# Kernel optimization log

Measured on AMD Instinct MI355X. Metric: run time of the kernel, lower is better.

Reference implementation:

```python
import jax, jax.numpy as jnp
import numpy as np

B, L, N, C = 8, 33600, 128, 80
ALPHA, BETA, TOPK, EPS = 1.0, 6.0, 13, 1e-9


def setup_inputs() -> dict:
    key = jax.random.key(0)
    ks = jax.random.split(key, 7)
    pred_scores = jax.random.uniform(ks[0], (B, L, C), jnp.float32)  # post-sigmoid scores
    pc = jax.random.uniform(ks[1], (B, L, 2), jnp.float32) * 1024.0
    pwh = jax.random.uniform(ks[2], (B, L, 2), jnp.float32) * 128.0 + 8.0
    pred_boxes = jnp.concatenate([pc - pwh / 2, pc + pwh / 2], axis=-1)  # xyxy
    gc = jax.random.uniform(ks[3], (B, N, 2), jnp.float32) * 1024.0
    gwh = jax.random.uniform(ks[4], (B, N, 2), jnp.float32) * 256.0 + 16.0
    gt_boxes = jnp.concatenate([gc - gwh / 2, gc + gwh / 2], axis=-1)  # xyxy
    anchor_points = jax.random.uniform(ks[5], (1, L, 2), jnp.float32) * 1024.0
    gt_labels = jax.random.randint(ks[6], (B, N, 1), 0, C).astype(jnp.int64)
    # last quarter of GT slots are padding
    pad_gt_mask = (jnp.arange(N)[None, :, None] < 96).astype(jnp.float32)
    pad_gt_mask = jnp.broadcast_to(pad_gt_mask, (B, N, 1))
    return {"pred_scores": pred_scores, "pred_boxes": pred_boxes,
            "anchor_points": anchor_points, "gt_labels": gt_labels,
            "gt_boxes": gt_boxes, "pad_gt_mask": pad_gt_mask, "bg_index": C}


def _pairwise_iou(gt, pr):
    # gt: [B,N,4], pr: [B,L,4] xyxy -> iou [B,N,L]
    lt = jnp.maximum(gt[:, :, None, :2], pr[:, None, :, :2])
    rb = jnp.minimum(gt[:, :, None, 2:], pr[:, None, :, 2:])
    wh = jnp.clip(rb - lt, 0.0)
    inter = wh[..., 0] * wh[..., 1]
    area_g = ((gt[..., 2] - gt[..., 0]) * (gt[..., 3] - gt[..., 1]))[:, :, None]
    area_p = ((pr[..., 2] - pr[..., 0]) * (pr[..., 3] - pr[..., 1]))[:, None, :]
    iou = inter / (area_g + area_p - inter + EPS)
    iou = jnp.where(iou > 1.0 + EPS, 0.0, iou)
    return jnp.clip(jnp.nan_to_num(iou), 0.0, 1.0)


def reference(pred_scores, pred_boxes, anchor_points, gt_labels, gt_boxes, pad_gt_mask, bg_index):
    b, l, c = pred_scores.shape
    n = gt_boxes.shape[1]
    iou = _pairwise_iou(gt_boxes, pred_boxes)  # [B,N,L]

    # spatial containment of anchor points in horizontal gt boxes -> [B,N,L]
    pts = anchor_points[0]  # [L,2]
    spatial = ((pts[None, None, :, 0] >= gt_boxes[:, :, None, 0]) &
               (pts[None, None, :, 0] <= gt_boxes[:, :, None, 2]) &
               (pts[None, None, :, 1] >= gt_boxes[:, :, None, 1]) &
               (pts[None, None, :, 1] <= gt_boxes[:, :, None, 3]))

    # gather per-GT class scores: class_scores[b,n,l] = pred_scores[b,l,label[b,n]]
    lbl = jnp.clip(gt_labels[..., 0], 0, c - 1)  # [B,N]
    ps_t = jnp.transpose(pred_scores, (0, 2, 1))  # [B,C,L]
    class_scores = jnp.take_along_axis(ps_t, jnp.broadcast_to(lbl[:, :, None], (b, n, l)), axis=1)

    align = (class_scores ** ALPHA) * (iou ** BETA)  # [B,N,L]

    # top-k per GT over anchors
    k = min(TOPK, l)
    s = align * spatial.astype(align.dtype)
    _, topk_idx = jax.lax.top_k(s, k)  # [B,N,k]
    bidx = jnp.arange(b)[:, None, None]
    gidx = jnp.arange(n)[None, :, None]
    topk_mask = jnp.zeros((b, n, l), bool).at[bidx, gidx, topk_idx].set(True)
    topk_mask = topk_mask & (pad_gt_mask[..., 0] > 0)[:, :, None]

    positive = topk_mask.astype(align.dtype) * spatial.astype(align.dtype) * pad_gt_mask

    # conflict resolution: anchors matched to >1 GT keep only the best-IoU GT
    conflict = positive.sum(axis=1) > 1  # [B,L]
    best_gt = jnp.argmax(iou, axis=1)  # [B,L]
    best_mask = (jnp.arange(n)[None, :, None] == best_gt[:, None, :])  # [B,N,L]
    positive = jnp.where(conflict[:, None, :], positive * best_mask.astype(positive.dtype), positive)

    has_assign = positive.sum(axis=1) > 0  # [B,L]
    gt_idx = jnp.argmax(positive, axis=1)  # [B,L]
    assigned_labels = jnp.take_along_axis(gt_labels[..., 0], gt_idx, axis=1)  # [B,L]
    assigned_labels = jnp.where(has_assign, assigned_labels, bg_index)
    assigned_boxes = jnp.take_along_axis(gt_boxes, jnp.broadcast_to(gt_idx[:, :, None], (b, l, 4)), axis=1)

    masked_align = align * positive
    max_align = masked_align.max(axis=-1, keepdims=True)  # [B,N,1]
    max_iou = (iou * positive).max(axis=-1, keepdims=True)  # [B,N,1]
    norm_align = masked_align / (max_align + EPS) * max_iou
    norm_factor = norm_align.max(axis=1)  # [B,L]
    # scatter score at assigned class; bg labels (== C) one-hot to all-zero row
    assigned_scores = jax.nn.one_hot(assigned_labels, c, dtype=pred_scores.dtype)
    assigned_scores = assigned_scores * (norm_factor * has_assign.astype(norm_factor.dtype))[:, :, None]
    return assigned_labels, assigned_boxes, assigned_scores
```

## Files before the change

kernel.cpp:

```cpp
#include <hip/hip_runtime.h>
#include <cstdint>
#include <cstddef>

#define B_DIM 8
#define L_DIM 33600
#define N_DIM 128
#define C_DIM 80
#define K_TOP 13
#define EPS_F 1e-9f
#define NCH2 66
#define SEGSZ 32

typedef float f32x4 __attribute__((ext_vector_type(4)));

__device__ __forceinline__ float iou_pair(float g0, float g1, float g2, float g3,
                                          float p0, float p1, float p2, float p3) {
    float ltx = fmaxf(g0, p0), lty = fmaxf(g1, p1);
    float rbx = fminf(g2, p2), rby = fminf(g3, p3);
    float wx = fmaxf(__fsub_rn(rbx, ltx), 0.0f);
    float wy = fmaxf(__fsub_rn(rby, lty), 0.0f);
    float inter = __fmul_rn(wx, wy);
    float ag = __fmul_rn(__fsub_rn(g2, g0), __fsub_rn(g3, g1));
    float ap = __fmul_rn(__fsub_rn(p2, p0), __fsub_rn(p3, p1));
    float den = __fadd_rn(__fsub_rn(__fadd_rn(ag, ap), inter), EPS_F);
    float iou = __fdiv_rn(inter, den);
    if (iou > 1.0f) iou = 0.0f;
    iou = fminf(fmaxf(iou, 0.0f), 1.0f);
    return iou;
}

__device__ __forceinline__ unsigned long long make_key(double s, int l) {
    unsigned long long sb = (unsigned long long)__double_as_longlong(s);
    return (sb & 0xFFFFFFFFFFFF0000ull) | (unsigned long long)(0xFFFF - l);
}

__device__ __forceinline__ void nt_store4(float4 v, float4* p) {
    __builtin_nontemporal_store(*(f32x4*)&v, (f32x4*)p);
}

__global__ __launch_bounds__(256) void k_push(
    const float* __restrict__ pts, const float* __restrict__ pbox,
    const float* __restrict__ gbox, const float* __restrict__ gpad,
    const int* __restrict__ glbl, const float* __restrict__ psc,
    int* __restrict__ scount, unsigned long long* __restrict__ bucket,
    ulonglong2* __restrict__ posb2,
    float* __restrict__ maxal, float* __restrict__ maxio)
{
    const int chunk = blockIdx.x, b = blockIdx.y, t = threadIdx.x;
    __shared__ float4 gb[N_DIM];
    __shared__ int    gli[N_DIM];
    __shared__ int    lcnt[N_DIM];
    if (t < N_DIM) {
        float4 g = reinterpret_cast<const float4*>(gbox)[(size_t)b * N_DIM + t];
        if (gpad[b * N_DIM + t] <= 0.0f) g = make_float4(3e38f, 3e38f, -3e38f, -3e38f);
        gb[t] = g;
        gli[t] = min(max(glbl[b * N_DIM + t], 0), C_DIM - 1);
        lcnt[t] = 0;
        if (chunk == 0) { maxal[b * N_DIM + t] = 0.0f; maxio[b * N_DIM + t] = 0.0f; }
    }
    __syncthreads();

    const float* psb = psc + (size_t)b * L_DIM * C_DIM;
    const float4* pbb = reinterpret_cast<const float4*>(pbox) + (size_t)b * L_DIM;
    const int l0 = chunk * 512 + t, l1 = l0 + 256;
    const bool v0 = (l0 < L_DIM), v1 = (l1 < L_DIM);
    float a0x = -3e38f, a0y = -3e38f, a1x = -3e38f, a1y = -3e38f;
    float4 pb0 = make_float4(0, 0, 0, 0), pb1 = make_float4(0, 0, 0, 0);
    if (v0) {
        posb2[(size_t)b * L_DIM + l0] = make_ulonglong2(0ull, 0ull);
        const float2 ap = reinterpret_cast<const float2*>(pts)[l0];
        a0x = ap.x; a0y = ap.y;
        pb0 = pbb[l0];
    }
    if (v1) {
        posb2[(size_t)b * L_DIM + l1] = make_ulonglong2(0ull, 0ull);
        const float2 ap = reinterpret_cast<const float2*>(pts)[l1];
        a1x = ap.x; a1y = ap.y;
        pb1 = pbb[l1];
    }

    unsigned long long m0a = 0ull, m1a = 0ull, m0b = 0ull, m1b = 0ull;
    for (int n = 0; n < N_DIM; ++n) {
        const float4 g = gb[n];
        bool i0 = (a0x >= g.x && a0x <= g.z && a0y >= g.y && a0y <= g.w);
        bool i1 = (a1x >= g.x && a1x <= g.z && a1y >= g.y && a1y <= g.w);
        if (n < 64) { m0a |= i0 ? (1ull << n) : 0ull;        m0b |= i1 ? (1ull << n) : 0ull; }
        else        { m1a |= i0 ? (1ull << (n - 64)) : 0ull; m1b |= i1 ? (1ull << (n - 64)) : 0ull; }
    }

    const size_t segbase = ((size_t)(b * N_DIM) * NCH2 + chunk) * SEGSZ;
    if (v0 && l0 >= 32) {
        unsigned long long m = m0a | (m1a << 0);
        m = m0a;
        while (m) {
            int n = __ffsll((long long)m) - 1; m &= m - 1;
            const float4 g = gb[n];
            float iou = iou_pair(g.x, g.y, g.z, g.w, pb0.x, pb0.y, pb0.z, pb0.w);
            if (iou > 0.0f) {
                float cs = psb[(size_t)l0 * C_DIM + gli[n]];
                double d = (double)iou, d2 = d * d;
                unsigned long long key = make_key((double)cs * (d2 * d2 * d2), l0);
                int pos = atomicAdd(&lcnt[n], 1);
                if (pos < SEGSZ) bucket[segbase + (size_t)n * NCH2 * SEGSZ + pos] = key;
            }
        }
        m = m1a;
        while (m) {
            int n = __ffsll((long long)m) - 1; m &= m - 1;
            const float4 g = gb[n + 64];
            float iou = iou_pair(g.x, g.y, g.z, g.w, pb0.x, pb0.y, pb0.z, pb0.w);
            if (iou > 0.0f) {
                float cs = psb[(size_t)l0 * C_DIM + gli[n + 64]];
                double d = (double)iou, d2 = d * d;
                unsigned long long key = make_key((double)cs * (d2 * d2 * d2), l0);
                int pos = atomicAdd(&lcnt[n + 64], 1);
                if (pos < SEGSZ) bucket[segbase + (size_t)(n + 64) * NCH2 * SEGSZ + pos] = key;
            }
        }
    }
    if (v1) {
        unsigned long long m = m0b;
        while (m) {
            int n = __ffsll((long long)m) - 1; m &= m - 1;
            const float4 g = gb[n];
            float iou = iou_pair(g.x, g.y, g.z, g.w, pb1.x, pb1.y, pb1.z, pb1.w);
            if (iou > 0.0f) {
                float cs = psb[(size_t)l1 * C_DIM + gli[n]];
                double d = (double)iou, d2 = d * d;
                unsigned long long key = make_key((double)cs * (d2 * d2 * d2), l1);
                int pos = atomicAdd(&lcnt[n], 1);
                if (pos < SEGSZ) bucket[segbase + (size_t)n * NCH2 * SEGSZ + pos] = key;
            }
        }
        m = m1b;
        while (m) {
            int n = __ffsll((long long)m) - 1; m &= m - 1;
            const float4 g = gb[n + 64];
            float iou = iou_pair(g.x, g.y, g.z, g.w, pb1.x, pb1.y, pb1.z, pb1.w);
            if (iou > 0.0f) {
                float cs = psb[(size_t)l1 * C_DIM + gli[n + 64]];
                double d = (double)iou, d2 = d * d;
                unsigned long long key = make_key((double)cs * (d2 * d2 * d2), l1);
                int pos = atomicAdd(&lcnt[n + 64], 1);
                if (pos < SEGSZ) bucket[segbase + (size_t)(n + 64) * NCH2 * SEGSZ + pos] = key;
            }
        }
    }
    __syncthreads();

    if (t < N_DIM)
        scount[(b * N_DIM + t) * NCH2 + chunk] = min(lcnt[t], SEGSZ);
}

__global__ __launch_bounds__(256) void k_top13(
    const float* __restrict__ psc, const float* __restrict__ pbox,
    const float* __restrict__ pts, const int* __restrict__ glbl,
    const float* __restrict__ gbox, const float* __restrict__ gpad,
    const int* __restrict__ scount, const unsigned long long* __restrict__ bucket,
    unsigned long long* __restrict__ posbits)
{
    const int n = blockIdx.x, b = blockIdx.y, t = threadIdx.x;
    if (gpad[b * N_DIM + n] <= 0.0f) return;

    const float g0 = gbox[(b * N_DIM + n) * 4 + 0];
    const float g1 = gbox[(b * N_DIM + n) * 4 + 1];
    const float g2 = gbox[(b * N_DIM + n) * 4 + 2];
    const float g3 = gbox[(b * N_DIM + n) * 4 + 3];
    int lbl = glbl[b * N_DIM + n];
    lbl = min(max(lbl, 0), C_DIM - 1);
    const float* psb = psc + (size_t)b * L_DIM * C_DIM;
    const float* pbb = pbox + (size_t)b * L_DIM * 4;
    const int bn = b * N_DIM + n;

    __shared__ int pfx[NCH2 + 1];
    __shared__ int tmp[128];
    if (t < 128) tmp[t] = (t < NCH2) ? scount[bn * NCH2 + t] : 0;
    __syncthreads();
    #pragma unroll
    for (int off = 1; off < 128; off <<= 1) {
        int v = 0;
        if (t < 128) { v = tmp[t]; if (t >= off) v += tmp[t - off]; }
        __syncthreads();
        if (t < 128) tmp[t] = v;
        __syncthreads();
    }
    if (t < NCH2) pfx[t + 1] = tmp[t];
    if (t == 0) pfx[0] = 0;
    __syncthreads();
    const int nc = pfx[NCH2];
    const unsigned long long* seg = bucket + (size_t)bn * NCH2 * SEGSZ;

    unsigned long long key[K_TOP];
    #pragma unroll
    for (int k = 0; k < K_TOP; ++k) key[k] = 0ull;

    for (int i = t; i < nc + 32; i += 256) {
        unsigned long long ck;
        if (i < 32) {
            const int l = i;
            const float2 ap = reinterpret_cast<const float2*>(pts)[l];
            ck = (unsigned long long)(0xFFFF - l);
            if (ap.x >= g0 && ap.x <= g2 && ap.y >= g1 && ap.y <= g3) {
                const float4 pbv = reinterpret_cast<const float4*>(pbb)[l];
                float iou = iou_pair(g0, g1, g2, g3, pbv.x, pbv.y, pbv.z, pbv.w);
                if (iou > 0.0f) {
                    float cs = psb[(size_t)l * C_DIM + lbl];
                    double d = (double)iou, d2 = d * d;
                    ck = make_key((double)cs * (d2 * d2 * d2), l);
                }
            }
        } else {
            const int ci = i - 32;
            int lo = 0, hi = NCH2 - 1;
            while (lo < hi) { int mid = (lo + hi + 1) >> 1; if (pfx[mid] <= ci) lo = mid; else hi = mid - 1; }
            ck = seg[(size_t)lo * SEGSZ + (ci - pfx[lo])];
        }
        if (ck > key[K_TOP - 1]) {
            #pragma unroll
            for (int k = 0; k < K_TOP; ++k) {
                unsigned long long hi = key[k] > ck ? key[k] : ck;
                unsigned long long lo = key[k] > ck ? ck : key[k];
                key[k] = hi; ck = lo;
            }
        }
    }

    const int lane = t & 63, wid = t >> 6;
    __shared__ unsigned long long wl[4 * K_TOP];
    #pragma unroll 1
    for (int r = 0; r < K_TOP; ++r) {
        unsigned long long best = key[0];
        #pragma unroll
        for (int d = 1; d < 64; d <<= 1) {
            unsigned long long o = __shfl_xor(best, d, 64);
            best = o > best ? o : best;
        }
        if (best == 0ull) {
            if (lane == 0)
                for (int rr = r; rr < K_TOP; ++rr) wl[wid * K_TOP + rr] = 0ull;
            break;
        }
        if (key[0] == best) {
            #pragma unroll
            for (int k = 0; k < K_TOP - 1; ++k) key[k] = key[k + 1];
            key[K_TOP - 1] = 0ull;
        }
        if (lane == 0) wl[wid * K_TOP + r] = best;
    }
    __syncthreads();
    if (wid != 0) return;

    unsigned long long v = (lane < 4 * K_TOP) ? wl[lane] : 0ull;
    #pragma unroll 1
    for (int r = 0; r < K_TOP; ++r) {
        unsigned long long best = v;
        #pragma unroll
        for (int d = 1; d < 64; d <<= 1) {
            unsigned long long o = __shfl_xor(best, d, 64);
            best = o > best ? o : best;
        }
        if (v == best) v = 0ull;
        if (lane == 0) {
            int win = 0xFFFF - (int)(best & 0xFFFFull);
            atomicOr(&posbits[((size_t)b * L_DIM + win) * 2 + (n >> 6)],
                     1ULL << (n & 63));
        }
    }
}

__global__ __launch_bounds__(256) void k_assign(
    const float* __restrict__ psc, const float* __restrict__ pbox,
    const float* __restrict__ pts,
    const int* __restrict__ glbl, const float* __restrict__ gbox,
    const unsigned long long* __restrict__ posbits,
    const int* __restrict__ bgp,
    float* __restrict__ out_lab, float* __restrict__ out_box,
    int* __restrict__ fin_out, float* __restrict__ alat,
    float* __restrict__ maxal, float* __restrict__ maxio)
{
    const int b = blockIdx.y, t = threadIdx.x;
    const int l = blockIdx.x * 256 + t;
    __shared__ float4 gb[N_DIM];
    __shared__ int    gl[N_DIM];
    __shared__ int    qlist[256];
    __shared__ unsigned long long qp0[256], qp1[256];
    __shared__ int    qn;
    if (t == 0) qn = 0;
    if (t < N_DIM) {
        gb[t] = reinterpret_cast<const float4*>(gbox)[(size_t)b * N_DIM + t];
        gl[t] = glbl[b * N_DIM + t];
    }
    __syncthreads();

    if (l < L_DIM) {
        const size_t bl = (size_t)b * L_DIM + l;
        const unsigned long long w0 = posbits[bl * 2 + 0];
        const unsigned long long w1 = posbits[bl * 2 + 1];
        unsigned long long p0 = 0ull, p1 = 0ull;
        if (w0 | w1) {
            const float2 ap = reinterpret_cast<const float2*>(pts)[l];
            unsigned long long m = w0;
            while (m) {
                int n = __ffsll((long long)m) - 1; m &= m - 1;
                float4 g = gb[n];
                if (ap.x >= g.x && ap.x <= g.z && ap.y >= g.y && ap.y <= g.w)
                    p0 |= 1ull << n;
            }
            m = w1;
            while (m) {
                int n = __ffsll((long long)m) - 1; m &= m - 1;
                float4 g = gb[n + 64];
                if (ap.x >= g.x && ap.x <= g.z && ap.y >= g.y && ap.y <= g.w)
                    p1 |= 1ull << n;
            }
        }
        const int pcnt = __popcll(p0) + __popcll(p1);

        if (pcnt <= 1) {
            int fin = (pcnt == 1) ? (p0 ? (__ffsll(p0) - 1) : (64 + __ffsll(p1) - 1)) : -1;
            __builtin_nontemporal_store((fin >= 0) ? (float)gl[fin] : (float)bgp[0], &out_lab[bl]);
            int gidx = (fin >= 0) ? fin : 0;
            nt_store4(gb[gidx], &reinterpret_cast<float4*>(out_box)[bl]);
            fin_out[bl] = fin;
            if (fin >= 0) {
                const float4 pb = reinterpret_cast<const float4*>(pbox)[bl];
                float4 g = gb[fin];
                float iou = iou_pair(g.x, g.y, g.z, g.w, pb.x, pb.y, pb.z, pb.w);
                int lb = min(max(gl[fin], 0), C_DIM - 1);
                float cs = psc[bl * C_DIM + lb];
                float al = cs * powf(iou, 6.0f);
                alat[bl] = al;
                atomicMax((int*)&maxal[b * N_DIM + fin], __float_as_int(al));
                atomicMax((int*)&maxio[b * N_DIM + fin], __float_as_int(iou));
            }
        } else {
            int qi = atomicAdd(&qn, 1);
            qlist[qi] = l; qp0[qi] = p0; qp1[qi] = p1;
        }
    }
    __syncthreads();

    const int lane = t & 63, wid = t >> 6;
    const int nq = qn;
    for (int i = wid; i < nq; i += 4) {
        const int ql = qlist[i];
        const size_t bl = (size_t)b * L_DIM + ql;
        const float4 pb = reinterpret_cast<const float4*>(pbox)[bl];
        float4 gA = gb[lane];
        float4 gB = gb[lane + 64];
        float iouA = iou_pair(gA.x, gA.y, gA.z, gA.w, pb.x, pb.y, pb.z, pb.w);
        float iouB = iou_pair(gB.x, gB.y, gB.z, gB.w, pb.x, pb.y, pb.z, pb.w);
        unsigned long long kA = ((unsigned long long)__float_as_uint(iouA) << 32)
                              | (unsigned long long)(0xFFFFFFFFu - (unsigned)lane);
        unsigned long long kB = ((unsigned long long)__float_as_uint(iouB) << 32)
                              | (unsigned long long)(0xFFFFFFFFu - (unsigned)(lane + 64));
        unsigned long long k = kA > kB ? kA : kB;
        #pragma unroll
        for (int d = 1; d < 64; d <<= 1) {
            unsigned long long o = __shfl_xor(k, d, 64);
            k = o > k ? o : k;
        }
        if (lane == 0) {
            int bestn = (int)(0xFFFFFFFFu - (unsigned)(k & 0xFFFFFFFFull));
            float bestiou = __uint_as_float((unsigned)(k >> 32));
            const unsigned long long p0 = qp0[i], p1 = qp1[i];
            bool posbest = (bestn < 64) ? ((p0 >> bestn) & 1ull) : ((p1 >> (bestn - 64)) & 1ull);
            int fin = posbest ? bestn : -1;
            __builtin_nontemporal_store((fin >= 0) ? (float)gl[fin] : (float)bgp[0], &out_lab[bl]);
            int gidx = (fin >= 0) ? fin : 0;
            nt_store4(gb[gidx], &reinterpret_cast<float4*>(out_box)[bl]);
            fin_out[bl] = fin;
            if (fin >= 0) {
                int lb = min(max(gl[fin], 0), C_DIM - 1);
                float cs = psc[bl * C_DIM + lb];
                float al = cs * powf(bestiou, 6.0f);
                alat[bl] = al;
                atomicMax((int*)&maxal[b * N_DIM + fin], __float_as_int(al));
                atomicMax((int*)&maxio[b * N_DIM + fin], __float_as_int(bestiou));
            }
        }
    }
}

__global__ __launch_bounds__(256) void k_out(
    const int* __restrict__ fin_out, const float* __restrict__ alat,
    const float* __restrict__ maxal, const float* __restrict__ maxio,
    const int* __restrict__ glbl,
    float* __restrict__ outs)
{
    const int APB = 16;
    const int a0 = blockIdx.x * APB;
    const int t = threadIdx.x;
    __shared__ float snf[APB];
    __shared__ int   scl[APB];
    if (t < APB) {
        int a = a0 + t;
        float v = 0.0f; int c = -1;
        if (a < B_DIM * L_DIM) {
            int b = a / L_DIM;
            int fin = fin_out[a];
            if (fin >= 0) {
                v = alat[a] / (maxal[b * N_DIM + fin] + EPS_F) * maxio[b * N_DIM + fin];
                c = glbl[b * N_DIM + fin];
            }
        }
        snf[t] = v; scl[t] = c;
    }
    __syncthreads();
    float4* out4 = reinterpret_cast<float4*>(outs);
    for (int j = t; j < APB * 20; j += 256) {
        int ai = j / 20;
        int a = a0 + ai;
        if (a >= B_DIM * L_DIM) continue;
        int c0 = (j - ai * 20) * 4;
        float v = snf[ai]; int cl = scl[ai];
        float4 o;
        o.x = (c0 + 0 == cl) ? v : 0.0f;
        o.y = (c0 + 1 == cl) ? v : 0.0f;
        o.z = (c0 + 2 == cl) ? v : 0.0f;
        o.w = (c0 + 3 == cl) ? v : 0.0f;
        nt_store4(o, &out4[(size_t)a * 20 + (j - ai * 20)]);
    }
}

extern "C" void kernel_launch(void* const* d_in, const int* in_sizes, int n_in,
                              void* d_out, int out_size, void* d_ws, size_t ws_size,
                              hipStream_t stream)
{
    const float* psc  = (const float*)d_in[0];
    const float* pbox = (const float*)d_in[1];
    const float* pts  = (const float*)d_in[2];
    const int*   glbl = (const int*)d_in[3];
    const float* gbox = (const float*)d_in[4];
    const float* gpad = (const float*)d_in[5];
    const int*   bgp  = (const int*)d_in[6];

    const size_t P = (size_t)B_DIM * L_DIM * 2 * sizeof(unsigned long long);
    char* w = (char*)d_ws;
    unsigned long long* posbits = (unsigned long long*)w;
    float* maxal = (float*)(w + P);
    float* maxio = (float*)(w + P + 4096);
    int*   scount = (int*) (w + P + 8192);
    int*   fin   = (int*)  (w + P + 8192 + 270336);
    float* alat  = (float*)(w + P + 8192 + 270336 + 1075200);
    unsigned long long* bucket = (unsigned long long*)(w + P + 8192 + 270336 + 2 * 1075200);

    float* out_lab = (float*)d_out;
    float* out_box = out_lab + (size_t)B_DIM * L_DIM;
    float* out_sc  = out_box + (size_t)B_DIM * L_DIM * 4;

    k_push<<<dim3(NCH2, B_DIM), dim3(256), 0, stream>>>(
        pts, pbox, gbox, gpad, glbl, psc, scount, bucket, (ulonglong2*)posbits, maxal, maxio);
    k_top13<<<dim3(N_DIM, B_DIM), dim3(256), 0, stream>>>(
        psc, pbox, pts, glbl, gbox, gpad, scount, bucket, posbits);
    k_assign<<<dim3((L_DIM + 255) / 256, B_DIM), dim3(256), 0, stream>>>(
        psc, pbox, pts, glbl, gbox, posbits, bgp,
        out_lab, out_box, fin, alat, maxal, maxio);
    k_out<<<dim3((B_DIM * L_DIM + 15) / 16), dim3(256), 0, stream>>>(
        fin, alat, maxal, maxio, glbl, out_sc);
}
```

Baseline: 76.40 us.

## Map one GT per wavefront in top-k and grid-stride the score output kernel

The top-13 kernel now assigns each (batch, GT) pair to a single 64-lane wavefront, four per block. Each wave compacts its bucket segments into shared memory with an atomic cursor, replacing the block-wide prefix scan, binary search and two-level cross-wave merge. The output kernel switches from one block per 16-anchor tile to a fixed 2048-block grid-stride loop. This cuts block launches and barriers, but it caps candidates at 352 per GT and leaves fewer threads per GT for the insertion sort.

```diff
diff --git a/kernel.cpp b/kernel.cpp
--- a/kernel.cpp
+++ b/kernel.cpp
@@ -10,6 +10,7 @@
 #define EPS_F 1e-9f
 #define NCH2 66
 #define SEGSZ 32
+#define WBUF 352
 
 typedef float f32x4 __attribute__((ext_vector_type(4)));
 
@@ -90,8 +91,7 @@
 
     const size_t segbase = ((size_t)(b * N_DIM) * NCH2 + chunk) * SEGSZ;
     if (v0 && l0 >= 32) {
-        unsigned long long m = m0a | (m1a << 0);
-        m = m0a;
+        unsigned long long m = m0a;
         while (m) {
             int n = __ffsll((long long)m) - 1; m &= m - 1;
             const float4 g = gb[n];
@@ -159,9 +159,31 @@
     const int* __restrict__ scount, const unsigned long long* __restrict__ bucket,
     unsigned long long* __restrict__ posbits)
 {
-    const int n = blockIdx.x, b = blockIdx.y, t = threadIdx.x;
-    if (gpad[b * N_DIM + n] <= 0.0f) return;
-
+    const int t = threadIdx.x, lane = t & 63, wid = t >> 6;
+    const int bn = blockIdx.x * 4 + wid;
+    const int b = bn >> 7, n = bn & 127;
+    const bool active = (gpad[b * N_DIM + n] > 0.0f);
+
+    __shared__ unsigned long long buf[4][WBUF];
+    __shared__ int wq[4];
+    if (lane == 0) wq[wid] = 0;
+    __builtin_amdgcn_wave_barrier();
+
+    if (active) {
+        for (int s = lane; s < NCH2; s += 64) {
+            int c = scount[bn * NCH2 + s];
+            if (c > 0) {
+                int pos = atomicAdd(&wq[wid], c);
+                const unsigned long long* seg = bucket + ((size_t)bn * NCH2 + s) * SEGSZ;
+                for (int j = 0; j < c; ++j)
+                    if (pos + j < WBUF) buf[wid][pos + j] = seg[j];
+            }
+        }
+    }
+    __syncthreads();
+    if (!active) return;
+
+    const int nc = min(wq[wid], WBUF);
     const float g0 = gbox[(b * N_DIM + n) * 4 + 0];
     const float g1 = gbox[(b * N_DIM + n) * 4 + 1];
     const float g2 = gbox[(b * N_DIM + n) * 4 + 2];
@@ -170,51 +192,28 @@
     lbl = min(max(lbl, 0), C_DIM - 1);
     const float* psb = psc + (size_t)b * L_DIM * C_DIM;
     const float* pbb = pbox + (size_t)b * L_DIM * 4;
-    const int bn = b * N_DIM + n;
-
-    __shared__ int pfx[NCH2 + 1];
-    __shared__ int tmp[128];
-    if (t < 128) tmp[t] = (t < NCH2) ? scount[bn * NCH2 + t] : 0;
-    __syncthreads();
-    #pragma unroll
-    for (int off = 1; off < 128; off <<= 1) {
-        int v = 0;
-        if (t < 128) { v = tmp[t]; if (t >= off) v += tmp[t - off]; }
-        __syncthreads();
-        if (t < 128) tmp[t] = v;
-        __syncthreads();
-    }
-    if (t < NCH2) pfx[t + 1] = tmp[t];
-    if (t == 0) pfx[0] = 0;
-    __syncthreads();
-    const int nc = pfx[NCH2];
-    const unsigned long long* seg = bucket + (size_t)bn * NCH2 * SEGSZ;
 
     unsigned long long key[K_TOP];
     #pragma unroll
     for (int k = 0; k < K_TOP; ++k) key[k] = 0ull;
 
-    for (int i = t; i < nc + 32; i += 256) {
-        unsigned long long ck;
-        if (i < 32) {
-            const int l = i;
-            const float2 ap = reinterpret_cast<const float2*>(pts)[l];
-            ck = (unsigned long long)(0xFFFF - l);
-            if (ap.x >= g0 && ap.x <= g2 && ap.y >= g1 && ap.y <= g3) {
-                const float4 pbv = reinterpret_cast<const float4*>(pbb)[l];
-                float iou = iou_pair(g0, g1, g2, g3, pbv.x, pbv.y, pbv.z, pbv.w);
-                if (iou > 0.0f) {
-                    float cs = psb[(size_t)l * C_DIM + lbl];
-                    double d = (double)iou, d2 = d * d;
-                    ck = make_key((double)cs * (d2 * d2 * d2), l);
-                }
-            }
-        } else {
-            const int ci = i - 32;
-            int lo = 0, hi = NCH2 - 1;
-            while (lo < hi) { int mid = (lo + hi + 1) >> 1; if (pfx[mid] <= ci) lo = mid; else hi = mid - 1; }
-            ck = seg[(size_t)lo * SEGSZ + (ci - pfx[lo])];
-        }
+    if (lane < 32) {
+        const int l = lane;
+        const float2 ap = reinterpret_cast<const float2*>(pts)[l];
+        unsigned long long ck = (unsigned long long)(0xFFFF - l);
+        if (ap.x >= g0 && ap.x <= g2 && ap.y >= g1 && ap.y <= g3) {
+            const float4 pbv = reinterpret_cast<const float4*>(pbb)[l];
+            float iou = iou_pair(g0, g1, g2, g3, pbv.x, pbv.y, pbv.z, pbv.w);
+            if (iou > 0.0f) {
+                float cs = psb[(size_t)l * C_DIM + lbl];
+                double d = (double)iou, d2 = d * d;
+                ck = make_key((double)cs * (d2 * d2 * d2), l);
+            }
+        }
+        key[0] = ck;
+    }
+    for (int i = lane; i < nc; i += 64) {
+        unsigned long long ck = buf[wid][i];
         if (ck > key[K_TOP - 1]) {
             #pragma unroll
             for (int k = 0; k < K_TOP; ++k) {
@@ -225,8 +224,6 @@
         }
     }
 
-    const int lane = t & 63, wid = t >> 6;
-    __shared__ unsigned long long wl[4 * K_TOP];
     #pragma unroll 1
     for (int r = 0; r < K_TOP; ++r) {
         unsigned long long best = key[0];
@@ -235,31 +232,11 @@
             unsigned long long o = __shfl_xor(best, d, 64);
             best = o > best ? o : best;
         }
-        if (best == 0ull) {
-            if (lane == 0)
-                for (int rr = r; rr < K_TOP; ++rr) wl[wid * K_TOP + rr] = 0ull;
-            break;
-        }
-        if (key[0] == best) {
+        if (key[0] == best && best != 0ull) {
             #pragma unroll
             for (int k = 0; k < K_TOP - 1; ++k) key[k] = key[k + 1];
             key[K_TOP - 1] = 0ull;
         }
-        if (lane == 0) wl[wid * K_TOP + r] = best;
-    }
-    __syncthreads();
-    if (wid != 0) return;
-
-    unsigned long long v = (lane < 4 * K_TOP) ? wl[lane] : 0ull;
-    #pragma unroll 1
-    for (int r = 0; r < K_TOP; ++r) {
-        unsigned long long best = v;
-        #pragma unroll
-        for (int d = 1; d < 64; d <<= 1) {
-            unsigned long long o = __shfl_xor(best, d, 64);
-            best = o > best ? o : best;
-        }
-        if (v == best) v = 0ull;
         if (lane == 0) {
             int win = 0xFFFF - (int)(best & 0xFFFFull);
             atomicOr(&posbits[((size_t)b * L_DIM + win) * 2 + (n >> 6)],
@@ -389,37 +366,42 @@
     float* __restrict__ outs)
 {
     const int APB = 16;
-    const int a0 = blockIdx.x * APB;
+    const int NTILES = (B_DIM * L_DIM + APB - 1) / APB;
     const int t = threadIdx.x;
     __shared__ float snf[APB];
     __shared__ int   scl[APB];
-    if (t < APB) {
-        int a = a0 + t;
-        float v = 0.0f; int c = -1;
-        if (a < B_DIM * L_DIM) {
-            int b = a / L_DIM;
-            int fin = fin_out[a];
-            if (fin >= 0) {
-                v = alat[a] / (maxal[b * N_DIM + fin] + EPS_F) * maxio[b * N_DIM + fin];
-                c = glbl[b * N_DIM + fin];
-            }
-        }
-        snf[t] = v; scl[t] = c;
-    }
-    __syncthreads();
     float4* out4 = reinterpret_cast<float4*>(outs);
-    for (int j = t; j < APB * 20; j += 256) {
-        int ai = j / 20;
-        int a = a0 + ai;
-        if (a >= B_DIM * L_DIM) continue;
-        int c0 = (j - ai * 20) * 4;
-        float v = snf[ai]; int cl = scl[ai];
-        float4 o;
-        o.x = (c0 + 0 == cl) ? v : 0.0f;
-        o.y = (c0 + 1 == cl) ? v : 0.0f;
-        o.z = (c0 + 2 == cl) ? v : 0.0f;
-        o.w = (c0 + 3 == cl) ? v : 0.0f;
-        nt_store4(o, &out4[(size_t)a * 20 + (j - ai * 20)]);
+
+    for (int tile = blockIdx.x; tile < NTILES; tile += 2048) {
+        const int a0 = tile * APB;
+        __syncthreads();
+        if (t < APB) {
+            int a = a0 + t;
+            float v = 0.0f; int c = -1;
+            if (a < B_DIM * L_DIM) {
+                int b = a / L_DIM;
+                int fin = fin_out[a];
+                if (fin >= 0) {
+                    v = alat[a] / (maxal[b * N_DIM + fin] + EPS_F) * maxio[b * N_DIM + fin];
+                    c = glbl[b * N_DIM + fin];
+                }
+            }
+            snf[t] = v; scl[t] = c;
+        }
+        __syncthreads();
+        for (int j = t; j < APB * 20; j += 256) {
+            int ai = j / 20;
+            int a = a0 + ai;
+            if (a >= B_DIM * L_DIM) continue;
+            int c0 = (j - ai * 20) * 4;
+            float v = snf[ai]; int cl = scl[ai];
+            float4 o;
+            o.x = (c0 + 0 == cl) ? v : 0.0f;
+            o.y = (c0 + 1 == cl) ? v : 0.0f;
+            o.z = (c0 + 2 == cl) ? v : 0.0f;
+            o.w = (c0 + 3 == cl) ? v : 0.0f;
+            nt_store4(o, &out4[(size_t)a * 20 + (j - ai * 20)]);
+        }
     }
 }
 
@@ -451,11 +433,11 @@
 
     k_push<<<dim3(NCH2, B_DIM), dim3(256), 0, stream>>>(
         pts, pbox, gbox, gpad, glbl, psc, scount, bucket, (ulonglong2*)posbits, maxal, maxio);
-    k_top13<<<dim3(N_DIM, B_DIM), dim3(256), 0, stream>>>(
+    k_top13<<<dim3(256), dim3(256), 0, stream>>>(
         psc, pbox, pts, glbl, gbox, gpad, scount, bucket, posbits);
     k_assign<<<dim3((L_DIM + 255) / 256, B_DIM), dim3(256), 0, stream>>>(
         psc, pbox, pts, glbl, gbox, posbits, bgp,
         out_lab, out_box, fin, alat, maxal, maxio);
-    k_out<<<dim3((B_DIM * L_DIM + 15) / 16), dim3(256), 0, stream>>>(
+    k_out<<<dim3(2048), dim3(256), 0, stream>>>(
         fin, alat, maxal, maxio, glbl, out_sc);
 }
```

Result: no change. 75.37 us (-1.4%).
